# Optimization experiments

Measured on AMD Instinct MI355X. Metric: run time of the kernel, lower is better.

Reference implementation:

```python
import jax, jax.numpy as jnp
import numpy as np

N_NODES = 50000
N_EDGES = 800000
D_FEAT = 64
IN_DIM = 1 + 2 * D_FEAT  # 129
FC_DIMS = [128, 64, 1]


def setup_inputs() -> dict:
    key = jax.random.key(0)
    ks = jax.random.split(key, 10)
    x = jax.random.normal(ks[0], (N_NODES, D_FEAT), dtype=jnp.float32)
    edge_index = jax.random.randint(ks[1], (2, N_EDGES), 0, N_NODES, dtype=jnp.int64)
    edge_weight = jax.random.uniform(ks[2], (N_EDGES, 1), dtype=jnp.float32)
    # MLP params (Linear: y = x @ W.T + b), Kaiming-ish scale
    dims = [IN_DIM] + FC_DIMS
    W1 = jax.random.normal(ks[3], (dims[1], dims[0]), dtype=jnp.float32) / np.sqrt(dims[0])
    b1 = jnp.zeros((dims[1],), dtype=jnp.float32)
    W2 = jax.random.normal(ks[4], (dims[2], dims[1]), dtype=jnp.float32) / np.sqrt(dims[1])
    b2 = jnp.zeros((dims[2],), dtype=jnp.float32)
    W3 = jax.random.normal(ks[5], (dims[3], dims[2]), dtype=jnp.float32) / np.sqrt(dims[2])
    b3 = jnp.zeros((dims[3],), dtype=jnp.float32)
    return {"x": x, "edge_index": edge_index, "edge_weight": edge_weight,
            "W1": W1, "b1": b1, "W2": W2, "b2": b2, "W3": W3, "b3": b3}


def reference(x, edge_index, edge_weight, W1, b1, W2, b2, W3, b3):
    # Gather source/target node features per edge: [E, d]
    src = x[edge_index[0]]
    tgt = x[edge_index[1]]
    # Concat [edge_weight | src | tgt] -> [E, 1 + 2d]
    h = jnp.concatenate([edge_weight, src, tgt], axis=1)
    # MLP (dropout is None / eval; last layer dim==1 -> no ReLU)
    h = jax.nn.relu(h @ W1.T + b1)
    h = jax.nn.relu(h @ W2.T + b2)
    return h @ W3.T + b3  # [E, 1] new edge weights
```

## Files before the change

kernel.cpp:

```cpp
#include <hip/hip_runtime.h>

typedef _Float16 half8 __attribute__((ext_vector_type(8)));
typedef _Float16 half4_t __attribute__((ext_vector_type(4)));
typedef float floatx4 __attribute__((ext_vector_type(4)));

__device__ __forceinline__ int swz(int row, int col) {
    return row * 128 + (col ^ ((row & 7) << 3));
}

__global__ __launch_bounds__(256) void prep_kernel(
    const float* __restrict__ x,
    const float* __restrict__ W1, const float* __restrict__ W2,
    const float* __restrict__ b1, const float* __restrict__ b2,
    const float* __restrict__ W3,
    _Float16* __restrict__ wsh, float* __restrict__ pf,
    _Float16* __restrict__ xh, int n_x8)
{
    int b = blockIdx.x;
    if (b < 96) {
        int tid = b * 256 + threadIdx.x;
        if (tid < 16384) {
            int c = tid >> 9, r = tid & 511;
            int L = r >> 3, jj = r & 7;
            int mt = c >> 2, kb = c & 3;
            int n = mt * 16 + (L & 15);
            int k = kb * 32 + (L >> 4) * 8 + jj;
            wsh[tid] = (_Float16)W1[n * 129 + 1 + k];
        } else {
            int t = tid - 16384;
            int c = t >> 9, r = t & 511;
            int L = r >> 3, jj = r & 7;
            int it = c >> 2, kb = c & 3;
            int i = it * 16 + (L & 15);
            int j = kb * 32 + (L >> 4) * 8 + jj;
            wsh[tid] = (_Float16)W2[i * 128 + j];
        }
    } else if (b == 96) {
        for (int i = threadIdx.x; i < 384; i += 256) {
            float v;
            if (i < 128)      v = b1[i];
            else if (i < 256) v = W1[(i - 128) * 129];
            else if (i < 320) v = b2[i - 256];
            else              v = W3[i - 320];
            pf[i] = v;
        }
    } else {
        int t2 = (b - 97) * 256 + threadIdx.x;
        if (t2 < n_x8) {
            const float4* p = (const float4*)(x + (size_t)t2 * 8);
            float4 v0 = p[0], v1 = p[1];
            half8 h = {(_Float16)v0.x, (_Float16)v0.y, (_Float16)v0.z, (_Float16)v0.w,
                       (_Float16)v1.x, (_Float16)v1.y, (_Float16)v1.z, (_Float16)v1.w};
            *(half8*)(xh + (size_t)t2 * 8) = h;
        }
    }
}

__global__ __launch_bounds__(256, 4) void edge_mlp_kernel(
    const _Float16* __restrict__ xh,
    const int* __restrict__ ei,
    const float* __restrict__ ew,
    const float* __restrict__ b3,
    const _Float16* __restrict__ wf,
    const float* __restrict__ pf,
    float* __restrict__ out, int E)
{
    __shared__ __align__(16) _Float16 hA[128 * 128];

    const int tid  = threadIdx.x;
    const int lane = tid & 63;
    const int wave = tid >> 6;
    const int lrow = lane & 15;
    const int quad = lane >> 4;
    const int e_blk = blockIdx.x * 128;

    int   eg[2];
    float ewv[2];
#pragma unroll
    for (int nt = 0; nt < 2; ++nt) {
        int e = e_blk + wave * 32 + nt * 16 + lrow;
        if (e >= E) e = E - 1;
        eg[nt] = e;
        ewv[nt] = ew[e];
    }
    half8 bfr[2][4];
#pragma unroll
    for (int nt = 0; nt < 2; ++nt) {
        int n0 = ei[eg[nt]];
        int n1 = ei[E + eg[nt]];
#pragma unroll
        for (int kb = 0; kb < 4; ++kb) {
            int node = (kb < 2) ? n0 : n1;
            bfr[nt][kb] = *(const half8*)(xh + (size_t)node * 64 + (kb & 1) * 32 + quad * 8);
        }
    }

#pragma unroll
    for (int mt = 0; mt < 8; ++mt) {
        half8 afr[4];
#pragma unroll
        for (int kb = 0; kb < 4; ++kb)
            afr[kb] = *(const half8*)(wf + (mt * 4 + kb) * 512 + lane * 8);
        int nb = mt * 16 + quad * 4;
        float4 b1v = *(const float4*)(pf + nb);
        float4 c0v = *(const float4*)(pf + 128 + nb);
#pragma unroll
        for (int nt = 0; nt < 2; ++nt) {
            floatx4 a = {0.f, 0.f, 0.f, 0.f};
#pragma unroll
            for (int kb = 0; kb < 4; ++kb)
                a = __builtin_amdgcn_mfma_f32_16x16x32_f16(afr[kb], bfr[nt][kb], a, 0, 0, 0);
            half4_t hv;
            {
                float v0 = a[0] + b1v.x + ewv[nt] * c0v.x;
                float v1 = a[1] + b1v.y + ewv[nt] * c0v.y;
                float v2 = a[2] + b1v.z + ewv[nt] * c0v.z;
                float v3 = a[3] + b1v.w + ewv[nt] * c0v.w;
                hv[0] = (_Float16)fmaxf(v0, 0.f);
                hv[1] = (_Float16)fmaxf(v1, 0.f);
                hv[2] = (_Float16)fmaxf(v2, 0.f);
                hv[3] = (_Float16)fmaxf(v3, 0.f);
            }
            int row = wave * 32 + nt * 16 + lrow;
            *(half4_t*)(&hA[swz(row, nb)]) = hv;
        }
    }
    __syncthreads();

    half8 b2fr[2][4];
#pragma unroll
    for (int nt = 0; nt < 2; ++nt) {
        int row = wave * 32 + nt * 16 + lrow;
#pragma unroll
        for (int kb = 0; kb < 4; ++kb)
            b2fr[nt][kb] = *(const half8*)(&hA[swz(row, kb * 32 + quad * 8)]);
    }

    const float b3v = b3[0];
    float tot[2] = {b3v, b3v};
#pragma unroll
    for (int it = 0; it < 4; ++it) {
        half8 a2[4];
#pragma unroll
        for (int kb = 0; kb < 4; ++kb)
            a2[kb] = *(const half8*)(wf + 16384 + (it * 4 + kb) * 512 + lane * 8);
        int ib = it * 16 + quad * 4;
        float4 b2v = *(const float4*)(pf + 256 + ib);
        float4 w3v = *(const float4*)(pf + 320 + ib);
#pragma unroll
        for (int nt = 0; nt < 2; ++nt) {
            floatx4 a = {0.f, 0.f, 0.f, 0.f};
#pragma unroll
            for (int kb = 0; kb < 4; ++kb)
                a = __builtin_amdgcn_mfma_f32_16x16x32_f16(a2[kb], b2fr[nt][kb], a, 0, 0, 0);
            float p = fmaxf(a[0] + b2v.x, 0.f) * w3v.x;
            p      += fmaxf(a[1] + b2v.y, 0.f) * w3v.y;
            p      += fmaxf(a[2] + b2v.z, 0.f) * w3v.z;
            p      += fmaxf(a[3] + b2v.w, 0.f) * w3v.w;
            p += __shfl_xor(p, 16, 64);
            p += __shfl_xor(p, 32, 64);
            tot[nt] += p;
        }
    }

#pragma unroll
    for (int nt = 0; nt < 2; ++nt) {
        if (quad == 0) {
            int oe = e_blk + wave * 32 + nt * 16 + lrow;
            if (oe < E) out[oe] = tot[nt];
        }
    }
}

extern "C" void kernel_launch(void* const* d_in, const int* in_sizes, int n_in,
                              void* d_out, int out_size, void* d_ws, size_t ws_size,
                              hipStream_t stream) {
    const float* x  = (const float*)d_in[0];
    const int*   ei = (const int*)d_in[1];
    const float* ew = (const float*)d_in[2];
    const float* W1 = (const float*)d_in[3];
    const float* b1 = (const float*)d_in[4];
    const float* W2 = (const float*)d_in[5];
    const float* b2 = (const float*)d_in[6];
    const float* W3 = (const float*)d_in[7];
    const float* b3 = (const float*)d_in[8];
    float* out = (float*)d_out;
    const int E = in_sizes[2];
    const int n_x = in_sizes[0];
    const int n_x8 = n_x / 8;

    _Float16* wsh = (_Float16*)d_ws;
    float*    pf  = (float*)((char*)d_ws + 49152);
    _Float16* xh  = (_Float16*)((char*)d_ws + 51200);

    int xblk = (n_x8 + 255) / 256;
    prep_kernel<<<97 + xblk, 256, 0, stream>>>(x, W1, W2, b1, b2, W3,
                                               wsh, pf, xh, n_x8);

    int nblk = (E + 127) / 128;
    edge_mlp_kernel<<<nblk, 256, 0, stream>>>(xh, ei, ew, b3, wsh, pf, out, E);
}
```

Baseline: 156.5 us.

## Precompute per-node layer-1 projections and gather them per edge

The first linear layer is split by linearity. Each node's source and target projections (W1_src·x + b1 and W1_tgt·x) are computed once per node with MFMA in the prep kernel, and each edge then gathers and adds two 128-wide fp16 rows plus the edge-weight term before ReLU. This replaces the per-edge 128x128 layer-1 GEMM and the shared-memory staging of its output with a per-node GEMM over 50k nodes. In exchange, each edge gathers 512 bytes instead of 256, the layer-1 sum and ReLU are done in fp16, and the prep kernel now writes a larger intermediate buffer.

```diff
diff --git a/kernel.cpp b/kernel.cpp
--- a/kernel.cpp
+++ b/kernel.cpp
@@ -3,172 +3,169 @@
 typedef _Float16 half8 __attribute__((ext_vector_type(8)));
 typedef _Float16 half4_t __attribute__((ext_vector_type(4)));
 typedef float floatx4 __attribute__((ext_vector_type(4)));
-
-__device__ __forceinline__ int swz(int row, int col) {
-    return row * 128 + (col ^ ((row & 7) << 3));
-}
 
 __global__ __launch_bounds__(256) void prep_kernel(
     const float* __restrict__ x,
     const float* __restrict__ W1, const float* __restrict__ W2,
     const float* __restrict__ b1, const float* __restrict__ b2,
     const float* __restrict__ W3,
-    _Float16* __restrict__ wsh, float* __restrict__ pf,
-    _Float16* __restrict__ xh, int n_x8)
+    _Float16* __restrict__ w2f, float* __restrict__ pf,
+    _Float16* __restrict__ c0h,
+    _Float16* __restrict__ Ps, _Float16* __restrict__ Pt,
+    int n_nodes, int nb_gemm)
 {
-    int b = blockIdx.x;
-    if (b < 96) {
-        int tid = b * 256 + threadIdx.x;
-        if (tid < 16384) {
-            int c = tid >> 9, r = tid & 511;
-            int L = r >> 3, jj = r & 7;
-            int mt = c >> 2, kb = c & 3;
-            int n = mt * 16 + (L & 15);
-            int k = kb * 32 + (L >> 4) * 8 + jj;
-            wsh[tid] = (_Float16)W1[n * 129 + 1 + k];
-        } else {
-            int t = tid - 16384;
+    const int b = blockIdx.x;
+    const int tid = threadIdx.x;
+
+    if (b < nb_gemm) {
+        __shared__ __align__(16) _Float16 sW[16384];
+        for (int c = tid; c < 4096; c += 256) {
+            int lin = c * 4;
+            int n = lin >> 7, kk = lin & 127;
+            const float* wp = W1 + n * 129 + 1 + kk;
+            float w0 = wp[0], w1 = wp[1], w2 = wp[2], w3 = wp[3];
+            int mt = n >> 4, kb = kk >> 5;
+            int L = (n & 15) + (((kk >> 3) & 3) << 4);
+            int pos = (mt * 4 + kb) * 512 + L * 8 + (kk & 7);
+            half4_t h = {(_Float16)w0, (_Float16)w1, (_Float16)w2, (_Float16)w3};
+            *(half4_t*)(&sW[pos]) = h;
+        }
+        __syncthreads();
+
+        const int lane = tid & 63, wave = tid >> 6;
+        const int lrow = lane & 15, quad = lane >> 4;
+        const int tile = b * 4 + wave;
+        if (tile * 16 < n_nodes) {
+            int node = tile * 16 + lrow;
+            if (node >= n_nodes) node = n_nodes - 1;
+            const float* xr = x + (size_t)node * 64 + quad * 8;
+            float4 x0 = *(const float4*)(xr);
+            float4 x1 = *(const float4*)(xr + 4);
+            float4 x2 = *(const float4*)(xr + 32);
+            float4 x3 = *(const float4*)(xr + 36);
+            half8 bx0 = {(_Float16)x0.x, (_Float16)x0.y, (_Float16)x0.z, (_Float16)x0.w,
+                         (_Float16)x1.x, (_Float16)x1.y, (_Float16)x1.z, (_Float16)x1.w};
+            half8 bx1 = {(_Float16)x2.x, (_Float16)x2.y, (_Float16)x2.z, (_Float16)x2.w,
+                         (_Float16)x3.x, (_Float16)x3.y, (_Float16)x3.z, (_Float16)x3.w};
+#pragma unroll
+            for (int mt = 0; mt < 8; ++mt) {
+                half8 a0 = *(const half8*)(&sW[(mt * 4 + 0) * 512 + lane * 8]);
+                half8 a1 = *(const half8*)(&sW[(mt * 4 + 1) * 512 + lane * 8]);
+                half8 a2 = *(const half8*)(&sW[(mt * 4 + 2) * 512 + lane * 8]);
+                half8 a3 = *(const half8*)(&sW[(mt * 4 + 3) * 512 + lane * 8]);
+                floatx4 ap = {0.f, 0.f, 0.f, 0.f};
+                floatx4 at = {0.f, 0.f, 0.f, 0.f};
+                ap = __builtin_amdgcn_mfma_f32_16x16x32_f16(a0, bx0, ap, 0, 0, 0);
+                ap = __builtin_amdgcn_mfma_f32_16x16x32_f16(a1, bx1, ap, 0, 0, 0);
+                at = __builtin_amdgcn_mfma_f32_16x16x32_f16(a2, bx0, at, 0, 0, 0);
+                at = __builtin_amdgcn_mfma_f32_16x16x32_f16(a3, bx1, at, 0, 0, 0);
+                int nb = mt * 16 + quad * 4;
+                float4 b1v = *(const float4*)(b1 + nb);
+                half4_t hs, ht;
+                hs[0] = (_Float16)(ap[0] + b1v.x);
+                hs[1] = (_Float16)(ap[1] + b1v.y);
+                hs[2] = (_Float16)(ap[2] + b1v.z);
+                hs[3] = (_Float16)(ap[3] + b1v.w);
+                ht[0] = (_Float16)at[0];
+                ht[1] = (_Float16)at[1];
+                ht[2] = (_Float16)at[2];
+                ht[3] = (_Float16)at[3];
+                *(half4_t*)(Ps + (size_t)node * 128 + nb) = hs;
+                *(half4_t*)(Pt + (size_t)node * 128 + nb) = ht;
+            }
+        }
+    } else if (b < nb_gemm + 32) {
+        int t = (b - nb_gemm) * 256 + tid;
+        if (t < 8192) {
             int c = t >> 9, r = t & 511;
             int L = r >> 3, jj = r & 7;
             int it = c >> 2, kb = c & 3;
             int i = it * 16 + (L & 15);
             int j = kb * 32 + (L >> 4) * 8 + jj;
-            wsh[tid] = (_Float16)W2[i * 128 + j];
-        }
-    } else if (b == 96) {
-        for (int i = threadIdx.x; i < 384; i += 256) {
-            float v;
-            if (i < 128)      v = b1[i];
-            else if (i < 256) v = W1[(i - 128) * 129];
-            else if (i < 320) v = b2[i - 256];
-            else              v = W3[i - 320];
-            pf[i] = v;
+            w2f[t] = (_Float16)W2[i * 128 + j];
         }
     } else {
-        int t2 = (b - 97) * 256 + threadIdx.x;
-        if (t2 < n_x8) {
-            const float4* p = (const float4*)(x + (size_t)t2 * 8);
-            float4 v0 = p[0], v1 = p[1];
-            half8 h = {(_Float16)v0.x, (_Float16)v0.y, (_Float16)v0.z, (_Float16)v0.w,
-                       (_Float16)v1.x, (_Float16)v1.y, (_Float16)v1.z, (_Float16)v1.w};
-            *(half8*)(xh + (size_t)t2 * 8) = h;
-        }
+        if (tid < 64)            pf[tid] = b2[tid];
+        else if (tid < 128)      pf[tid] = W3[tid - 64];
+        else                     c0h[tid - 128] = (_Float16)W1[(tid - 128) * 129];
     }
 }
 
 __global__ __launch_bounds__(256, 4) void edge_mlp_kernel(
-    const _Float16* __restrict__ xh,
-    const int* __restrict__ ei,
-    const float* __restrict__ ew,
+    const _Float16* __restrict__ Ps, const _Float16* __restrict__ Pt,
+    const int* __restrict__ ei, const float* __restrict__ ew,
     const float* __restrict__ b3,
-    const _Float16* __restrict__ wf,
-    const float* __restrict__ pf,
+    const _Float16* __restrict__ w2f, const float* __restrict__ pf,
+    const _Float16* __restrict__ c0h,
     float* __restrict__ out, int E)
 {
-    __shared__ __align__(16) _Float16 hA[128 * 128];
-
     const int tid  = threadIdx.x;
     const int lane = tid & 63;
     const int wave = tid >> 6;
     const int lrow = lane & 15;
     const int quad = lane >> 4;
-    const int e_blk = blockIdx.x * 128;
-
-    int   eg[2];
-    float ewv[2];
+    const int e0 = blockIdx.x * 128 + wave * 32;
+
+    half8 c0f[4];
+#pragma unroll
+    for (int kb = 0; kb < 4; ++kb)
+        c0f[kb] = *(const half8*)(c0h + kb * 32 + quad * 8);
+
+    half8 bfr[2][4];
 #pragma unroll
     for (int nt = 0; nt < 2; ++nt) {
-        int e = e_blk + wave * 32 + nt * 16 + lrow;
-        if (e >= E) e = E - 1;
-        eg[nt] = e;
-        ewv[nt] = ew[e];
-    }
-    half8 bfr[2][4];
-#pragma unroll
-    for (int nt = 0; nt < 2; ++nt) {
-        int n0 = ei[eg[nt]];
-        int n1 = ei[E + eg[nt]];
+        int e = e0 + nt * 16 + lrow; if (e >= E) e = E - 1;
+        float ewf = ew[e];
+        int sn = ei[e];
+        int tn = ei[E + e];
+        const _Float16* psp = Ps + (size_t)sn * 128 + quad * 8;
+        const _Float16* ptp = Pt + (size_t)tn * 128 + quad * 8;
+        _Float16 eh = (_Float16)ewf;
+        half8 ev = {eh, eh, eh, eh, eh, eh, eh, eh};
+        half8 z  = {0, 0, 0, 0, 0, 0, 0, 0};
 #pragma unroll
         for (int kb = 0; kb < 4; ++kb) {
-            int node = (kb < 2) ? n0 : n1;
-            bfr[nt][kb] = *(const half8*)(xh + (size_t)node * 64 + (kb & 1) * 32 + quad * 8);
-        }
-    }
-
-#pragma unroll
-    for (int mt = 0; mt < 8; ++mt) {
-        half8 afr[4];
+            half8 ps = *(const half8*)(psp + kb * 32);
+            half8 pt = *(const half8*)(ptp + kb * 32);
+            half8 s = ps + pt;
+            s = s + ev * c0f[kb];
+            s = __builtin_elementwise_max(s, z);
+            bfr[nt][kb] = s;
+        }
+    }
+
+    const float b3v = b3[0];
+    float tot0 = b3v, tot1 = b3v;
+#pragma unroll
+    for (int it = 0; it < 4; ++it) {
+        half8 a2[4];
 #pragma unroll
         for (int kb = 0; kb < 4; ++kb)
-            afr[kb] = *(const half8*)(wf + (mt * 4 + kb) * 512 + lane * 8);
-        int nb = mt * 16 + quad * 4;
-        float4 b1v = *(const float4*)(pf + nb);
-        float4 c0v = *(const float4*)(pf + 128 + nb);
+            a2[kb] = *(const half8*)(w2f + (it * 4 + kb) * 512 + lane * 8);
+        int ib = it * 16 + quad * 4;
+        float4 b2v = *(const float4*)(pf + ib);
+        float4 w3v = *(const float4*)(pf + 64 + ib);
 #pragma unroll
         for (int nt = 0; nt < 2; ++nt) {
             floatx4 a = {0.f, 0.f, 0.f, 0.f};
 #pragma unroll
             for (int kb = 0; kb < 4; ++kb)
-                a = __builtin_amdgcn_mfma_f32_16x16x32_f16(afr[kb], bfr[nt][kb], a, 0, 0, 0);
-            half4_t hv;
-            {
-                float v0 = a[0] + b1v.x + ewv[nt] * c0v.x;
-                float v1 = a[1] + b1v.y + ewv[nt] * c0v.y;
-                float v2 = a[2] + b1v.z + ewv[nt] * c0v.z;
-                float v3 = a[3] + b1v.w + ewv[nt] * c0v.w;
-                hv[0] = (_Float16)fmaxf(v0, 0.f);
-                hv[1] = (_Float16)fmaxf(v1, 0.f);
-                hv[2] = (_Float16)fmaxf(v2, 0.f);
-                hv[3] = (_Float16)fmaxf(v3, 0.f);
-            }
-            int row = wave * 32 + nt * 16 + lrow;
-            *(half4_t*)(&hA[swz(row, nb)]) = hv;
-        }
-    }
-    __syncthreads();
-
-    half8 b2fr[2][4];
-#pragma unroll
-    for (int nt = 0; nt < 2; ++nt) {
-        int row = wave * 32 + nt * 16 + lrow;
-#pragma unroll
-        for (int kb = 0; kb < 4; ++kb)
-            b2fr[nt][kb] = *(const half8*)(&hA[swz(row, kb * 32 + quad * 8)]);
-    }
-
-    const float b3v = b3[0];
-    float tot[2] = {b3v, b3v};
-#pragma unroll
-    for (int it = 0; it < 4; ++it) {
-        half8 a2[4];
-#pragma unroll
-        for (int kb = 0; kb < 4; ++kb)
-            a2[kb] = *(const half8*)(wf + 16384 + (it * 4 + kb) * 512 + lane * 8);
-        int ib = it * 16 + quad * 4;
-        float4 b2v = *(const float4*)(pf + 256 + ib);
-        float4 w3v = *(const float4*)(pf + 320 + ib);
-#pragma unroll
-        for (int nt = 0; nt < 2; ++nt) {
-            floatx4 a = {0.f, 0.f, 0.f, 0.f};
-#pragma unroll
-            for (int kb = 0; kb < 4; ++kb)
-                a = __builtin_amdgcn_mfma_f32_16x16x32_f16(a2[kb], b2fr[nt][kb], a, 0, 0, 0);
+                a = __builtin_amdgcn_mfma_f32_16x16x32_f16(a2[kb], bfr[nt][kb], a, 0, 0, 0);
             float p = fmaxf(a[0] + b2v.x, 0.f) * w3v.x;
             p      += fmaxf(a[1] + b2v.y, 0.f) * w3v.y;
             p      += fmaxf(a[2] + b2v.z, 0.f) * w3v.z;
             p      += fmaxf(a[3] + b2v.w, 0.f) * w3v.w;
             p += __shfl_xor(p, 16, 64);
             p += __shfl_xor(p, 32, 64);
-            tot[nt] += p;
-        }
-    }
-
-#pragma unroll
-    for (int nt = 0; nt < 2; ++nt) {
-        if (quad == 0) {
-            int oe = e_blk + wave * 32 + nt * 16 + lrow;
-            if (oe < E) out[oe] = tot[nt];
-        }
+            if (nt == 0) tot0 += p; else tot1 += p;
+        }
+    }
+
+    if (quad == 0) {
+        int oe0 = e0 + lrow;
+        int oe1 = e0 + 16 + lrow;
+        if (oe0 < E) out[oe0] = tot0;
+        if (oe1 < E) out[oe1] = tot1;
     }
 }
 
@@ -187,16 +184,21 @@
     float* out = (float*)d_out;
     const int E = in_sizes[2];
     const int n_x = in_sizes[0];
-    const int n_x8 = n_x / 8;
-
-    _Float16* wsh = (_Float16*)d_ws;
-    float*    pf  = (float*)((char*)d_ws + 49152);
-    _Float16* xh  = (_Float16*)((char*)d_ws + 51200);
-
-    int xblk = (n_x8 + 255) / 256;
-    prep_kernel<<<97 + xblk, 256, 0, stream>>>(x, W1, W2, b1, b2, W3,
-                                               wsh, pf, xh, n_x8);
+    const int n_nodes = n_x / 64;
+
+    _Float16* w2f = (_Float16*)d_ws;
+    float*    pf  = (float*)((char*)d_ws + 16384);
+    _Float16* c0h = (_Float16*)((char*)d_ws + 16896);
+    _Float16* Ps  = (_Float16*)((char*)d_ws + 17152);
+    _Float16* Pt  = (_Float16*)((char*)d_ws + 17152 + (size_t)n_nodes * 256);
+
+    int tiles = (n_nodes + 15) / 16;
+    int nb_gemm = (tiles + 3) / 4;
+    prep_kernel<<<nb_gemm + 33, 256, 0, stream>>>(x, W1, W2, b1, b2, W3,
+                                                  w2f, pf, c0h, Ps, Pt,
+                                                  n_nodes, nb_gemm);
 
     int nblk = (E + 127) / 128;
-    edge_mlp_kernel<<<nblk, 256, 0, stream>>>(xh, ei, ew, b3, wsh, pf, out, E);
+    edge_mlp_kernel<<<nblk, 256, 0, stream>>>(Ps, Pt, ei, ew, b3,
+                                              w2f, pf, c0h, out, E);
 }
```

Result: slower. 159.8 us (+2.1%).
